# Kernel tuning notes

Hardware: AMD Instinct MI355X
Metric: run time of the kernel (lower is better)

The kernel has to match this reference:

```python
import jax, jax.numpy as jnp
import numpy as np

EPS = 1e-5  # torch LayerNorm default
B, S, D, H = 1, 2048, 512, 32
DH = D // H
DFF = 2 * D


def _ln(x, g, b):
    m = jnp.mean(x, -1, keepdims=True)
    v = jnp.var(x, -1, keepdims=True)
    return (x - m) * jax.lax.rsqrt(v + EPS) * g + b


def setup_inputs() -> dict:
    key = jax.random.key(0)
    ks = iter(jax.random.split(key, 24))
    sc = 1.0 / np.sqrt(D)

    def lin(k, din, dout):  # weight stored [in, out]; y = x @ W + b
        return jax.random.normal(k, (din, dout), jnp.float32) * (1.0 / np.sqrt(din))

    inp = {
        "x": jax.random.normal(next(ks), (B, S, D), jnp.float32),
        # outer pre-norm
        "ln0_g": jnp.ones((D,), jnp.float32), "ln0_b": jnp.zeros((D,), jnp.float32),
        # MultiHead per-branch LayerNorms (3 distinct param sets)
        "lnq_g": jnp.ones((D,), jnp.float32), "lnq_b": jnp.zeros((D,), jnp.float32),
        "lnk_g": jnp.ones((D,), jnp.float32), "lnk_b": jnp.zeros((D,), jnp.float32),
        "lnv_g": jnp.ones((D,), jnp.float32), "lnv_b": jnp.zeros((D,), jnp.float32),
        # QKV + output projections
        "Wq": lin(next(ks), D, D), "bq": jax.random.normal(next(ks), (D,), jnp.float32) * sc,
        "Wk": lin(next(ks), D, D), "bk": jax.random.normal(next(ks), (D,), jnp.float32) * sc,
        "Wv": lin(next(ks), D, D), "bv": jax.random.normal(next(ks), (D,), jnp.float32) * sc,
        "Wo": lin(next(ks), D, D), "bo": jax.random.normal(next(ks), (D,), jnp.float32) * sc,
        # FFN
        "lnf_g": jnp.ones((D,), jnp.float32), "lnf_b": jnp.zeros((D,), jnp.float32),
        "W1": lin(next(ks), D, DFF), "b1": jax.random.normal(next(ks), (DFF,), jnp.float32) * sc,
        "W2": lin(next(ks), DFF, D), "b2": jax.random.normal(next(ks), (D,), jnp.float32) * (1.0 / np.sqrt(DFF)),
    }
    return inp


def reference(x, ln0_g, ln0_b, lnq_g, lnq_b, lnk_g, lnk_b, lnv_g, lnv_b,
              Wq, bq, Wk, bk, Wv, bv, Wo, bo, lnf_g, lnf_b, W1, b1, W2, b2):
    # Encoder: x = norm(x); out = MHA(x,x,x) + x; x = out + FFN(out)
    xn = _ln(x, ln0_g, ln0_b)

    # --- MultiHead (dropout = identity, eval mode) ---
    q = _ln(xn, lnq_g, lnq_b) @ Wq + bq
    k = _ln(xn, lnk_g, lnk_b) @ Wk + bk
    v = _ln(xn, lnv_g, lnv_b) @ Wv + bv
    # [B,S,D] -> [B,H,S,DH]
    q = q.reshape(B, S, H, DH).transpose(0, 2, 1, 3)
    k = k.reshape(B, S, H, DH).transpose(0, 2, 1, 3)
    v = v.reshape(B, S, H, DH).transpose(0, 2, 1, 3)

    scores = jnp.einsum("bhqd,bhkd->bhqk", q, k) / (DH ** 0.5)
    causal = jnp.tril(jnp.ones((S, S), bool))  # make_mask: triu(k=1)==0
    scores = jnp.where(causal, scores, jnp.float32(-1e9))
    attn = jax.nn.softmax(scores, axis=-1)
    ctx = jnp.einsum("bhqk,bhkd->bhqd", attn, v)
    ctx = ctx.transpose(0, 2, 1, 3).reshape(B, S, D)
    mha = ctx @ Wo + bo

    out = mha + xn  # first residual

    # --- FFN branch: LN -> Linear(2D) -> ReLU -> Linear(D) -> ReLU ---
    h = jax.nn.relu(_ln(out, lnf_g, lnf_b) @ W1 + b1)
    ffn = jax.nn.relu(h @ W2 + b2)
    return out + ffn
```

## Files before the change

### kernel.cpp

```cpp
#include <hip/hip_runtime.h>

#define S 2048
#define D 512
#define NH 32
#define DHD 16
#define DFF 1024
#define EPS 1e-5f
#define C1 0.36067376022224085f

typedef unsigned short u16;
typedef __attribute__((ext_vector_type(8))) short short8;
typedef __attribute__((ext_vector_type(4))) float f32x4;
typedef __attribute__((ext_vector_type(16))) float f32x16;
typedef __attribute__((ext_vector_type(4))) unsigned short us4;

#define GL_LDS(gsrc, ldst)                                                   \
  __builtin_amdgcn_global_load_lds(                                          \
      (const __attribute__((address_space(1))) unsigned int*)(gsrc),         \
      (__attribute__((address_space(3))) unsigned int*)(ldst), 16, 0, 0)

static __device__ __forceinline__ u16 f2bf(float f) {
  union { float f; unsigned int i; } c; c.f = f;
  unsigned int x = c.i;
  return (u16)((x + 0x7fffu + ((x >> 16) & 1u)) >> 16);
}
static __device__ __forceinline__ float bf2f(u16 v) {
  union { unsigned int i; float f; } c; c.i = ((unsigned int)v) << 16;
  return c.f;
}

static __device__ __forceinline__ float tsum16(const float* p) {
  float a0 = p[0] + p[1], a1 = p[2] + p[3], a2 = p[4] + p[5], a3 = p[6] + p[7];
  float a4 = p[8] + p[9], a5 = p[10] + p[11], a6 = p[12] + p[13], a7 = p[14] + p[15];
  float b0 = a0 + a1, b1 = a2 + a3, b2 = a4 + a5, b3 = a6 + a7;
  return (b0 + b1) + (b2 + b3);
}

__global__ __launch_bounds__(256) void prologue_kernel(
    const float* __restrict__ x,
    const float* __restrict__ g0, const float* __restrict__ b0,
    const float* __restrict__ gq, const float* __restrict__ bq,
    const float* __restrict__ gk, const float* __restrict__ bk,
    const float* __restrict__ gv, const float* __restrict__ bv,
    float* __restrict__ xn, u16* __restrict__ qin, u16* __restrict__ kin,
    u16* __restrict__ vin,
    const float* __restrict__ Wq, const float* __restrict__ Wk,
    const float* __restrict__ Wv, const float* __restrict__ Wo,
    const float* __restrict__ W1, const float* __restrict__ W2,
    u16* __restrict__ Fq, u16* __restrict__ Fk,
    u16* __restrict__ Fv, u16* __restrict__ Fo,
    u16* __restrict__ F1, u16* __restrict__ F2) {
  int bz = blockIdx.x;
  int t = threadIdx.x;
  if (bz < 2048) {
    __shared__ float tile[32][33];
    const float* W;
    u16* F;
    int K, N, n0, k0;
    if (bz < 1024) {
      int wi = bz >> 8, tl = bz & 255;
      W = wi == 0 ? Wq : wi == 1 ? Wk : wi == 2 ? Wv : Wo;
      F = wi == 0 ? Fq : wi == 1 ? Fk : wi == 2 ? Fv : Fo;
      K = 512; N = 512;
      n0 = (tl & 15) * 32; k0 = (tl >> 4) * 32;
    } else if (bz < 1536) {
      int tl = bz - 1024;
      W = W1; F = F1; K = 512; N = 1024;
      n0 = (tl & 31) * 32; k0 = (tl >> 5) * 32;
    } else {
      int tl = bz - 1536;
      W = W2; F = F2; K = 1024; N = 512;
      n0 = (tl & 15) * 32; k0 = (tl >> 4) * 32;
    }
    int tx = t & 31, ty = t >> 5;
#pragma unroll
    for (int i = 0; i < 4; ++i)
      tile[ty + 8 * i][tx] = W[(size_t)(k0 + ty + 8 * i) * N + n0 + tx];
    __syncthreads();
    int k = k0 + tx;
    int kpart = ((k >> 3) & 1) * 32;
    int kj = k & 7;
#pragma unroll
    for (int i = 0; i < 4; ++i) {
      int n = n0 + ty + 8 * i;
      size_t I = (size_t)((n >> 5) * (K >> 4) + (k >> 4)) * 512 + ((n & 31) + kpart) * 8 + kj;
      F[I] = f2bf(tile[tx][ty + 8 * i]);
    }
    return;
  }
  int w = t >> 6, lane = t & 63;
  int row = (bz - 2048) * 4 + w;
  int c = lane * 8;
  const float* xr = x + (size_t)row * D + c;
  float4 xa = *(const float4*)xr;
  float4 xb = *(const float4*)(xr + 4);
  float a[8] = {xa.x, xa.y, xa.z, xa.w, xb.x, xb.y, xb.z, xb.w};
  float s = 0.0f, ss = 0.0f;
#pragma unroll
  for (int i = 0; i < 8; ++i) { s += a[i]; ss += a[i] * a[i]; }
#pragma unroll
  for (int m = 1; m <= 32; m <<= 1) { s += __shfl_xor(s, m); ss += __shfl_xor(ss, m); }
  float mean = s * (1.0f / D);
  float rs = rsqrtf(ss * (1.0f / D) - mean * mean + EPS);
  float4 ga = *(const float4*)(g0 + c), gb = *(const float4*)(g0 + c + 4);
  float4 ba = *(const float4*)(b0 + c), bb = *(const float4*)(b0 + c + 4);
  float gg[8] = {ga.x, ga.y, ga.z, ga.w, gb.x, gb.y, gb.z, gb.w};
  float bbv[8] = {ba.x, ba.y, ba.z, ba.w, bb.x, bb.y, bb.z, bb.w};
  float y[8];
  float s2 = 0.0f, ss2 = 0.0f;
#pragma unroll
  for (int i = 0; i < 8; ++i) {
    y[i] = (a[i] - mean) * rs * gg[i] + bbv[i];
    s2 += y[i]; ss2 += y[i] * y[i];
  }
  float* xo = xn + (size_t)row * D + c;
  *(float4*)xo = {y[0], y[1], y[2], y[3]};
  *(float4*)(xo + 4) = {y[4], y[5], y[6], y[7]};
#pragma unroll
  for (int m = 1; m <= 32; m <<= 1) { s2 += __shfl_xor(s2, m); ss2 += __shfl_xor(ss2, m); }
  float m2 = s2 * (1.0f / D);
  float rs2 = rsqrtf(ss2 * (1.0f / D) - m2 * m2 + EPS);
  float cn[8];
#pragma unroll
  for (int i = 0; i < 8; ++i) cn[i] = (y[i] - m2) * rs2;
  size_t o = (size_t)row * D + c;
#pragma unroll
  for (int br = 0; br < 3; ++br) {
    const float* gp = br == 0 ? gq : br == 1 ? gk : gv;
    const float* bp = br == 0 ? bq : br == 1 ? bk : bv;
    u16* op = br == 0 ? qin : br == 1 ? kin : vin;
    float4 g1 = *(const float4*)(gp + c), g2 = *(const float4*)(gp + c + 4);
    float4 b1 = *(const float4*)(bp + c), b2 = *(const float4*)(bp + c + 4);
    float gv2[8] = {g1.x, g1.y, g1.z, g1.w, g2.x, g2.y, g2.z, g2.w};
    float bv2[8] = {b1.x, b1.y, b1.z, b1.w, b2.x, b2.y, b2.z, b2.w};
    us4 o1, o2;
#pragma unroll
    for (int i = 0; i < 4; ++i) o1[i] = f2bf(cn[i] * gv2[i] + bv2[i]);
#pragma unroll
    for (int i = 0; i < 4; ++i) o2[i] = f2bf(cn[4 + i] * gv2[4 + i] + bv2[4 + i]);
    *(us4*)(op + o) = o1;
    *(us4*)(op + o + 4) = o2;
  }
}

__global__ __launch_bounds__(256) void ln2_kernel(
    const float* __restrict__ in, const float* __restrict__ g,
    const float* __restrict__ b, u16* __restrict__ out) {
  int w = threadIdx.x >> 6, lane = threadIdx.x & 63;
  int row = blockIdx.x * 4 + w;
  int c = lane * 8;
  const float* xr = in + (size_t)row * D + c;
  float4 xa = *(const float4*)xr;
  float4 xb = *(const float4*)(xr + 4);
  float a[8] = {xa.x, xa.y, xa.z, xa.w, xb.x, xb.y, xb.z, xb.w};
  float s = 0.0f, ss = 0.0f;
#pragma unroll
  for (int i = 0; i < 8; ++i) { s += a[i]; ss += a[i] * a[i]; }
#pragma unroll
  for (int m = 1; m <= 32; m <<= 1) { s += __shfl_xor(s, m); ss += __shfl_xor(ss, m); }
  float mean = s * (1.0f / D);
  float rs = rsqrtf(ss * (1.0f / D) - mean * mean + EPS);
  float4 ga = *(const float4*)(g + c), gb = *(const float4*)(g + c + 4);
  float4 ba = *(const float4*)(b + c), bb = *(const float4*)(b + c + 4);
  float gg[8] = {ga.x, ga.y, ga.z, ga.w, gb.x, gb.y, gb.z, gb.w};
  float bbv[8] = {ba.x, ba.y, ba.z, ba.w, bb.x, bb.y, bb.z, bb.w};
  us4 o1, o2;
#pragma unroll
  for (int i = 0; i < 4; ++i) o1[i] = f2bf((a[i] - mean) * rs * gg[i] + bbv[i]);
#pragma unroll
  for (int i = 0; i < 4; ++i) o2[i] = f2bf((a[4 + i] - mean) * rs * gg[4 + i] + bbv[4 + i]);
  *(us4*)(out + (size_t)row * D + c) = o1;
  *(us4*)(out + (size_t)row * D + c + 4) = o2;
}

static __device__ __forceinline__ void stageA32(const u16* __restrict__ A, int K,
                                                int m0, int kk, u16* As, int t) {
#pragma unroll
  for (int j = 0; j < 4; ++j) {
    int idx = t + j * 128;
    int r = idx >> 3, sl = idx & 7;
    GL_LDS(A + (size_t)(m0 + r) * K + kk + ((sl ^ (r & 7)) * 8), As + idx * 8);
  }
}

static __device__ __forceinline__ void gemm32_acc(
    const u16* __restrict__ A, const u16* __restrict__ Wf, int K, int m0,
    int n32, u16 (*As)[4096], f32x16& acc) {
  int t = threadIdx.x, w = t >> 6, lane = t & 63;
  int l31 = lane & 31, hi5 = lane >> 5;
  const u16* bp = Wf + (size_t)n32 * (K >> 4) * 512 + lane * 8;
  stageA32(A, K, m0, 0, As[0], t);
  short8 bcur[4], bnxt[4];
#pragma unroll
  for (int ks = 0; ks < 4; ++ks) bcur[ks] = *(const short8*)(bp + ks * 512);
  __syncthreads();
  int pb = 0;
  int arow = w * 32 + l31;
  int abase = arow * 64;
  for (int kk = 0; kk < K; kk += 64) {
    if (kk + 64 < K) {
      stageA32(A, K, m0, kk + 64, As[pb ^ 1], t);
      const u16* bp2 = bp + (size_t)(kk + 64) * 32;
#pragma unroll
      for (int ks = 0; ks < 4; ++ks) bnxt[ks] = *(const short8*)(bp2 + ks * 512);
    }
#pragma unroll
    for (int ks = 0; ks < 4; ++ks) {
      int slot = (ks * 2 + hi5) ^ (arow & 7);
      short8 af = *(const short8*)&As[pb][abase + slot * 8];
      acc = __builtin_amdgcn_mfma_f32_32x32x16_bf16(af, bcur[ks], acc, 0, 0, 0);
    }
    __syncthreads();
    pb ^= 1;
#pragma unroll
    for (int ks = 0; ks < 4; ++ks) bcur[ks] = bnxt[ks];
  }
}

template <bool RELU, bool RESID, bool OUTBF>
__global__ __launch_bounds__(128) void gemm_kernel(
    const u16* __restrict__ A, const u16* __restrict__ Wf,
    const float* __restrict__ bias, const float* __restrict__ resid,
    float* __restrict__ outf, u16* __restrict__ outb, int N, int K) {
  __shared__ u16 As[2][4096];
  int m0 = blockIdx.x * 64, n0 = blockIdx.y * 32;
  f32x16 acc = {};
  gemm32_acc(A, Wf, K, m0, blockIdx.y, As, acc);
  int t = threadIdx.x, w = t >> 6, lane = t & 63;
  int l31 = lane & 31, hi5 = lane >> 5;
  int col = n0 + l31;
  float bv = bias[col];
#pragma unroll
  for (int r = 0; r < 16; ++r) {
    int row = m0 + w * 32 + (r & 3) + 8 * (r >> 2) + 4 * hi5;
    float v = acc[r] + bv;
    if (RELU) v = fmaxf(v, 0.0f);
    if (RESID) v += resid[(size_t)row * N + col];
    if (OUTBF)
      outb[(size_t)row * N + col] = f2bf(v);
    else
      outf[(size_t)row * N + col] = v;
  }
}

__global__ __launch_bounds__(128) void gemm_qkv(
    const u16* __restrict__ a0, const u16* __restrict__ a1, const u16* __restrict__ a2,
    const u16* __restrict__ w0, const u16* __restrict__ w1, const u16* __restrict__ w2,
    const float* __restrict__ c0, const float* __restrict__ c1, const float* __restrict__ c2,
    u16* __restrict__ Qb, u16* __restrict__ KtG, u16* __restrict__ VtG) {
  __shared__ u16 As[2][4096];
  int z = blockIdx.z;
  const u16* A = z == 0 ? a0 : z == 1 ? a1 : a2;
  const u16* Wf = z == 0 ? w0 : z == 1 ? w1 : w2;
  const float* bias = z == 0 ? c0 : z == 1 ? c1 : c2;
  int m0 = blockIdx.x * 64, n0 = blockIdx.y * 32;
  f32x16 acc = {};
  gemm32_acc(A, Wf, D, m0, blockIdx.y, As, acc);
  int t = threadIdx.x, w = t >> 6, lane = t & 63;
  int l31 = lane & 31, hi5 = lane >> 5;
  int col = n0 + l31;
  float bv = bias[col];
  int h = col >> 4, d = col & 15;
  if (z == 2) {
#pragma unroll
    for (int rg = 0; rg < 4; ++rg) {
      int row = m0 + w * 32 + 8 * rg + 4 * hi5;
      us4 pk;
#pragma unroll
      for (int j = 0; j < 4; ++j) pk[j] = f2bf(acc[rg * 4 + j] + bv);
      int I = (((row >> 5) * 4 + ((row >> 3) & 3)) * 16 + d) * 8 + (row & 7);
      *(us4*)(VtG + (size_t)h * 32768 + I) = pk;
    }
  } else {
#pragma unroll
    for (int r = 0; r < 16; ++r) {
      int row = m0 + w * 32 + (r & 3) + 8 * (r >> 2) + 4 * hi5;
      float v = acc[r] + bv;
      if (z == 0) {
        Qb[(size_t)row * D + col] = f2bf(v * C1);
      } else {
        int I = (((row >> 5) * 2 + (d >> 3)) * 32 + (row & 31)) * 8 + (d & 7);
        KtG[(size_t)h * 32768 + I] = f2bf(v);
      }
    }
  }
}

__global__ __launch_bounds__(128) void attn_kernel(const u16* __restrict__ Qb,
                                                   const u16* __restrict__ KtG,
                                                   const u16* __restrict__ VtG,
                                                   u16* __restrict__ ctx,
                                                   u16* __restrict__ part) {
  __shared__ u16 Pl[2][2048];

  const int t = threadIdx.x, w = t >> 6, lane = t & 63;
  const int h = blockIdx.y;
  const int f = 143 - blockIdx.x;
  int g = (int)((sqrtf((float)(1 + 2 * f)) - 1.0f) * 0.5f);
  while (2 * (g + 1) * (g + 2) <= f) ++g;
  while (2 * g * (g + 1) > f) --g;
  const int fg = f - 2 * g * (g + 1);
  const int qt = 4 * g + fg / (g + 1);
  const int c = fg - (fg / (g + 1)) * (g + 1);
  const int t0 = 4 * c;
  const int t1 = (4 * c + 3 < qt) ? 4 * c + 3 : qt;

  const int q0w = qt * 64 + w * 32;
  const int lq = lane & 31, hi = lane >> 5;
  const int l16 = lane & 15, g4 = lane >> 4;

  short8 qf = *(const short8*)(Qb + (size_t)(q0w + lq) * D + h * DHD + hi * 8);
  const u16* kp = KtG + (size_t)h * 32768 + (size_t)t0 * 1024 + hi * 256 + lq * 8;
  const u16* vp = VtG + (size_t)h * 32768 + (size_t)t0 * 1024 + g4 * 128 + l16 * 8;

  f32x4 acc[2] = {};
  float Lrun = 0.0f;

  short8 kf0 = *(const short8*)kp;
  short8 kf1 = *(const short8*)(kp + 512);
  short8 vf0 = *(const short8*)vp;
  short8 vf1 = *(const short8*)(vp + 512);

  u16* Pw = &Pl[w][0];
  const int pwr = (lq >> 4) * 1024 + (lq & 15) * 8 + 4 * hi;
  const int prd = g4 * 128 + l16 * 8;

  for (int tt = t0; tt <= t1; ++tt) {
    const int kv0 = tt * 64;
    const bool v1 = (kv0 + 32) <= (q0w + 31);
    f32x16 z = {};
    f32x16 st0 = __builtin_amdgcn_mfma_f32_32x32x16_bf16(kf0, qf, z, 0, 0, 0);
    f32x16 st1 = z;
    if (v1) st1 = __builtin_amdgcn_mfma_f32_32x32x16_bf16(kf1, qf, z, 0, 0, 0);

    short8 nk0, nk1, nv0, nv1;
    const bool more = (tt < t1);
    if (more) {
      kp += 1024; vp += 1024;
      nk0 = *(const short8*)kp;
      nk1 = *(const short8*)(kp + 512);
      nv0 = *(const short8*)vp;
      nv1 = *(const short8*)(vp + 512);
    }

    float p0[16], p1[16];
    const int thr0 = q0w + lq - kv0 - 4 * hi;
    if (kv0 + 31 > q0w) {
#pragma unroll
      for (int r = 0; r < 16; ++r) {
        const int rc = (r & 3) + 8 * (r >> 2);
        p0[r] = (rc > thr0) ? -1e30f : st0[r];
      }
    } else {
#pragma unroll
      for (int r = 0; r < 16; ++r) p0[r] = st0[r];
    }
#pragma unroll
    for (int r = 0; r < 16; ++r) p0[r] = exp2f(p0[r]);
    float sum = tsum16(p0);
    if (v1) {
      const int thr1 = thr0 - 32;
      if (kv0 + 63 > q0w) {
#pragma unroll
        for (int r = 0; r < 16; ++r) {
          const int rc = (r & 3) + 8 * (r >> 2);
          p1[r] = (rc > thr1) ? -1e30f : st1[r];
        }
      } else {
#pragma unroll
        for (int r = 0; r < 16; ++r) p1[r] = st1[r];
      }
#pragma unroll
      for (int r = 0; r < 16; ++r) p1[r] = exp2f(p1[r]);
      sum += tsum16(p1);
    }
    sum += __shfl_xor(sum, 32);
    Lrun += sum;

#pragma unroll
    for (int k = 0; k < 4; ++k) {
      unsigned int w0, w1;
      asm("v_cvt_pk_bf16_f32 %0, %1, %2" : "=v"(w0) : "v"(p0[4 * k]), "v"(p0[4 * k + 1]));
      asm("v_cvt_pk_bf16_f32 %0, %1, %2" : "=v"(w1) : "v"(p0[4 * k + 2]), "v"(p0[4 * k + 3]));
      uint2 pv; pv.x = w0; pv.y = w1;
      *(uint2*)&Pw[(pwr + k * 128) ^ (k << 4)] = pv;
    }
    if (v1) {
#pragma unroll
      for (int k = 0; k < 4; ++k) {
        unsigned int w0, w1;
        asm("v_cvt_pk_bf16_f32 %0, %1, %2" : "=v"(w0) : "v"(p1[4 * k]), "v"(p1[4 * k + 1]));
        asm("v_cvt_pk_bf16_f32 %0, %1, %2" : "=v"(w1) : "v"(p1[4 * k + 2]), "v"(p1[4 * k + 3]));
        uint2 pv; pv.x = w0; pv.y = w1;
        *(uint2*)&Pw[(pwr + 512 + k * 128) ^ (k << 4)] = pv;
      }
    }

#pragma unroll
    for (int sx = 0; sx < 2; ++sx) {
      if (sx == 0 || v1) {
        short8 vf = sx ? vf1 : vf0;
#pragma unroll
        for (int sq = 0; sq < 2; ++sq) {
          short8 pf = *(const short8*)&Pw[(sq * 1024 + sx * 512 + prd) ^ (g4 << 4)];
          acc[sq] = __builtin_amdgcn_mfma_f32_16x16x32_bf16(pf, vf, acc[sq], 0, 0, 0);
        }
      }
    }

    if (more) { kf0 = nk0; kf1 = nk1; vf0 = nv0; vf1 = nv1; }
  }

  if (g == 0) {
#pragma unroll
    for (int sq = 0; sq < 2; ++sq)
#pragma unroll
      for (int r = 0; r < 4; ++r) {
        int qlr = sq * 16 + g4 * 4 + r;
        float lv = __shfl(Lrun, qlr);
        float inv = __builtin_amdgcn_rcpf(lv);
        ctx[(size_t)(q0w + qlr) * D + h * DHD + l16] = f2bf(acc[sq][r] * inv);
      }
  } else {
    const int pslot = 2 * g * (g + 1) + (qt - 4 * g) * (g + 1) - 4 + c;
    u16* ps = part + ((size_t)(h * 140 + pslot)) * 1280;
#pragma unroll
    for (int sq = 0; sq < 2; ++sq)
#pragma unroll
      for (int r = 0; r < 4; ++r) {
        int qlocal = w * 32 + sq * 16 + g4 * 4 + r;
        ps[qlocal * 20 + 2 + l16] = f2bf(acc[sq][r]);
      }
    if (hi == 0) {
      *(float*)(ps + (w * 32 + lq) * 20) = Lrun;
    }
  }
}

__global__ __launch_bounds__(64) void attn_merge(const u16* __restrict__ part,
                                                 u16* __restrict__ ctx) {
  int qt = 4 + blockIdx.x, h = blockIdx.y, tq = threadIdx.x;
  int g = qt >> 2, nc = g + 1;
  int base = 2 * g * (g + 1) + (qt - 4 * g) * (g + 1) - 4;
  const u16* bp = part + ((size_t)(h * 140 + base)) * 1280 + tq * 20;
  float L = 0.0f;
  float o[16];
#pragma unroll
  for (int d = 0; d < 16; ++d) o[d] = 0.0f;
  for (int c = 0; c < nc; ++c) {
    const u16* pr = bp + (size_t)c * 1280;
    L += *(const float*)pr;
#pragma unroll
    for (int k = 0; k < 4; ++k) {
      us4 ov = *(const us4*)(pr + 2 + 4 * k);
#pragma unroll
      for (int j = 0; j < 4; ++j) o[4 * k + j] += bf2f(ov[j]);
    }
  }
  float inv = 1.0f / L;
  int q = qt * 64 + tq;
  u16* op = ctx + (size_t)q * D + h * DHD;
#pragma unroll
  for (int k = 0; k < 4; ++k) {
    us4 pk;
#pragma unroll
    for (int j = 0; j < 4; ++j) pk[j] = f2bf(o[4 * k + j] * inv);
    *(us4*)(op + 4 * k) = pk;
  }
}

extern "C" void kernel_launch(void* const* d_in, const int* in_sizes, int n_in,
                              void* d_out, int out_size, void* d_ws, size_t ws_size,
                              hipStream_t stream) {
  const float* x = (const float*)d_in[0];
  const float* ln0_g = (const float*)d_in[1];
  const float* ln0_b = (const float*)d_in[2];
  const float* lnq_g = (const float*)d_in[3];
  const float* lnq_b = (const float*)d_in[4];
  const float* lnk_g = (const float*)d_in[5];
  const float* lnk_b = (const float*)d_in[6];
  const float* lnv_g = (const float*)d_in[7];
  const float* lnv_b = (const float*)d_in[8];
  const float* Wq = (const float*)d_in[9];
  const float* bq = (const float*)d_in[10];
  const float* Wk = (const float*)d_in[11];
  const float* bk = (const float*)d_in[12];
  const float* Wv = (const float*)d_in[13];
  const float* bv = (const float*)d_in[14];
  const float* Wo = (const float*)d_in[15];
  const float* bo = (const float*)d_in[16];
  const float* lnf_g = (const float*)d_in[17];
  const float* lnf_b = (const float*)d_in[18];
  const float* W1 = (const float*)d_in[19];
  const float* b1 = (const float*)d_in[20];
  const float* W2 = (const float*)d_in[21];
  const float* b2 = (const float*)d_in[22];

  char* wsp = (char*)d_ws;
  size_t off = 0;
  auto alloc = [&](size_t bytes) -> void* {
    void* p = wsp + off;
    off += (bytes + 255) & ~(size_t)255;
    return p;
  };
  float* xn = (float*)alloc((size_t)S * D * 4);
  u16* Qb = (u16*)alloc((size_t)S * D * 2);
  u16* ctx = (u16*)alloc((size_t)S * D * 2);
  u16* KtG = (u16*)alloc((size_t)S * D * 2);
  u16* VtG = (u16*)alloc((size_t)S * D * 2);
  u16* WfQ = (u16*)alloc((size_t)D * D * 2);
  u16* WfK = (u16*)alloc((size_t)D * D * 2);
  u16* WfV = (u16*)alloc((size_t)D * D * 2);
  u16* WfO = (u16*)alloc((size_t)D * D * 2);
  u16* Wf1 = (u16*)alloc((size_t)D * DFF * 2);
  u16* Wf2 = (u16*)alloc((size_t)DFF * D * 2);
  char* regB = (char*)alloc((size_t)15 * 1024 * 1024);
  u16* qin = (u16*)regB;
  u16* kin = (u16*)(regB + (size_t)S * D * 2);
  u16* vin = (u16*)(regB + (size_t)S * D * 4);
  u16* part = (u16*)regB;
  float* outb = (float*)regB;
  u16* lnf = (u16*)(regB + (size_t)S * D * 4);
  u16* hbuf = (u16*)(regB + (size_t)S * D * 6);

  prologue_kernel<<<dim3(2560), 256, 0, stream>>>(
      x, ln0_g, ln0_b, lnq_g, lnq_b, lnk_g, lnk_b, lnv_g, lnv_b, xn, qin, kin, vin,
      Wq, Wk, Wv, Wo, W1, W2, WfQ, WfK, WfV, WfO, Wf1, Wf2);

  gemm_qkv<<<dim3(S / 64, D / 32, 3), 128, 0, stream>>>(
      qin, kin, vin, WfQ, WfK, WfV, bq, bk, bv, Qb, KtG, VtG);

  attn_kernel<<<dim3(144, NH), 128, 0, stream>>>(Qb, KtG, VtG, ctx, part);

  attn_merge<<<dim3(28, NH), 64, 0, stream>>>(part, ctx);

  gemm_kernel<false, true, false><<<dim3(S / 64, D / 32), 128, 0, stream>>>(
      ctx, WfO, bo, xn, outb, nullptr, D, D);

  ln2_kernel<<<S / 4, 256, 0, stream>>>(outb, lnf_g, lnf_b, lnf);

  gemm_kernel<true, false, true><<<dim3(S / 64, DFF / 32), 128, 0, stream>>>(
      lnf, Wf1, b1, nullptr, nullptr, hbuf, DFF, D);

  gemm_kernel<true, true, false><<<dim3(S / 64, D / 32), 128, 0, stream>>>(
      hbuf, Wf2, b2, outb, (float*)d_out, nullptr, D, DFF);

  (void)in_sizes; (void)n_in; (void)out_size; (void)ws_size;
}
```

Before: 88.28 us.

## Triple-buffer GEMM A tiles with prefetch distance two and one barrier per step

The shared GEMM main loop moves from double-buffered LDS staging to a three-slot ring. A and B tiles are now prefetched two K-steps ahead, and explicit s_waitcnt vmcnt waits plus a single s_barrier per iteration replace the two __syncthreads. The aim is to hide more global-load latency behind the MFMA work and cut barrier overhead. The cost is 50% more LDS per block and extra B-fragment registers, which may lower occupancy.

```diff
diff --git a/kernel.cpp b/kernel.cpp
--- a/kernel.cpp
+++ b/kernel.cpp
@@ -190,30 +190,38 @@
   int l31 = lane & 31, hi5 = lane >> 5;
   const u16* bp = Wf + (size_t)n32 * (K >> 4) * 512 + lane * 8;
   stageA32(A, K, m0, 0, As[0], t);
-  short8 bcur[4], bnxt[4];
-#pragma unroll
-  for (int ks = 0; ks < 4; ++ks) bcur[ks] = *(const short8*)(bp + ks * 512);
-  __syncthreads();
-  int pb = 0;
+  stageA32(A, K, m0, 64, As[1], t);
+  short8 bc[4], bn1[4], bn2[4];
+#pragma unroll
+  for (int ks = 0; ks < 4; ++ks) bc[ks] = *(const short8*)(bp + ks * 512);
+#pragma unroll
+  for (int ks = 0; ks < 4; ++ks) bn1[ks] = *(const short8*)(bp + 64 * 32 + ks * 512);
   int arow = w * 32 + l31;
   int abase = arow * 64;
+  int b = 0;
   for (int kk = 0; kk < K; kk += 64) {
     if (kk + 64 < K) {
-      stageA32(A, K, m0, kk + 64, As[pb ^ 1], t);
-      const u16* bp2 = bp + (size_t)(kk + 64) * 32;
-#pragma unroll
-      for (int ks = 0; ks < 4; ++ks) bnxt[ks] = *(const short8*)(bp2 + ks * 512);
+      asm volatile("s_waitcnt vmcnt(4)" ::: "memory");
+    } else {
+      asm volatile("s_waitcnt vmcnt(0)" ::: "memory");
+    }
+    __builtin_amdgcn_s_barrier();
+    if (kk + 128 < K) {
+      int b2i = b + 2 >= 3 ? b - 1 : b + 2;
+      stageA32(A, K, m0, kk + 128, As[b2i], t);
+      const u16* bp2 = bp + (size_t)(kk + 128) * 32;
+#pragma unroll
+      for (int ks = 0; ks < 4; ++ks) bn2[ks] = *(const short8*)(bp2 + ks * 512);
     }
 #pragma unroll
     for (int ks = 0; ks < 4; ++ks) {
       int slot = (ks * 2 + hi5) ^ (arow & 7);
-      short8 af = *(const short8*)&As[pb][abase + slot * 8];
-      acc = __builtin_amdgcn_mfma_f32_32x32x16_bf16(af, bcur[ks], acc, 0, 0, 0);
-    }
-    __syncthreads();
-    pb ^= 1;
-#pragma unroll
-    for (int ks = 0; ks < 4; ++ks) bcur[ks] = bnxt[ks];
+      short8 af = *(const short8*)&As[b][abase + slot * 8];
+      acc = __builtin_amdgcn_mfma_f32_32x32x16_bf16(af, bc[ks], acc, 0, 0, 0);
+    }
+#pragma unroll
+    for (int ks = 0; ks < 4; ++ks) { bc[ks] = bn1[ks]; bn1[ks] = bn2[ks]; }
+    b = b == 2 ? 0 : b + 1;
   }
 }
 
@@ -222,7 +230,7 @@
     const u16* __restrict__ A, const u16* __restrict__ Wf,
     const float* __restrict__ bias, const float* __restrict__ resid,
     float* __restrict__ outf, u16* __restrict__ outb, int N, int K) {
-  __shared__ u16 As[2][4096];
+  __shared__ u16 As[3][4096];
   int m0 = blockIdx.x * 64, n0 = blockIdx.y * 32;
   f32x16 acc = {};
   gemm32_acc(A, Wf, K, m0, blockIdx.y, As, acc);
@@ -248,7 +256,7 @@
     const u16* __restrict__ w0, const u16* __restrict__ w1, const u16* __restrict__ w2,
     const float* __restrict__ c0, const float* __restrict__ c1, const float* __restrict__ c2,
     u16* __restrict__ Qb, u16* __restrict__ KtG, u16* __restrict__ VtG) {
-  __shared__ u16 As[2][4096];
+  __shared__ u16 As[3][4096];
   int z = blockIdx.z;
   const u16* A = z == 0 ? a0 : z == 1 ? a1 : a2;
   const u16* Wf = z == 0 ? w0 : z == 1 ? w1 : w2;
```

Measured after the change: 88.42 us. No clear change (+0.2%).
